# Kernel tuning notes

Hardware: AMD Instinct MI355X
Metric: run time of the kernel (lower is better)

## Reference

```python
import jax, jax.numpy as jnp
import numpy as np

D_MODEL = 1024
NHEAD = 16
HEAD_DIM = D_MODEL // NHEAD


def setup_inputs() -> dict:
    key = jax.random.key(0)
    ks = jax.random.split(key, 9)
    s = 0.02
    x = jax.random.normal(ks[0], (2, 2048, D_MODEL), dtype=jnp.float32)
    Wq = jax.random.normal(ks[1], (D_MODEL, D_MODEL), dtype=jnp.float32) * s
    bq = jnp.zeros((D_MODEL,), jnp.float32)
    Wk = jax.random.normal(ks[2], (D_MODEL, D_MODEL), dtype=jnp.float32) * s
    bk = jnp.zeros((D_MODEL,), jnp.float32)
    Wv = jax.random.normal(ks[3], (D_MODEL, D_MODEL), dtype=jnp.float32) * s
    bv = jnp.zeros((D_MODEL,), jnp.float32)
    Wo = jax.random.normal(ks[4], (D_MODEL, D_MODEL), dtype=jnp.float32) * s
    bo = jnp.zeros((D_MODEL,), jnp.float32)
    return {"x": x, "Wq": Wq, "bq": bq, "Wk": Wk, "bk": bk,
            "Wv": Wv, "bv": bv, "Wo": Wo, "bo": bo}


def _rope(x, sin, cos):
    # x: [B, L, H, Dh]; rotate-half as in the torch module
    half = x.shape[-1] // 2
    x1, x2 = x[..., :half], x[..., half:]
    rotated = jnp.concatenate([-x2, x1], axis=-1)
    return x * cos + rotated * sin


def reference(x, Wq, bq, Wk, bk, Wv, bv, Wo, bo):
    B, L, D = x.shape
    H, Dh = NHEAD, HEAD_DIM
    q = (x @ Wq.T + bq).reshape(B, L, H, Dh)
    k = (x @ Wk.T + bk).reshape(B, L, H, Dh)
    v = (x @ Wv.T + bv).reshape(B, L, H, Dh)

    inv_freq = 1.0 / (10000.0 ** (jnp.arange(0, Dh, 2, dtype=jnp.float32) / Dh))
    t = jnp.arange(L, dtype=jnp.float32)
    freqs = jnp.einsum('i,j->ij', t, inv_freq)          # [L, Dh/2]
    emb = jnp.concatenate([freqs, freqs], axis=-1)      # [L, Dh]
    cos = jnp.cos(emb)[None, :, None, :]
    sin = jnp.sin(emb)[None, :, None, :]

    q = _rope(q, sin, cos)
    k = _rope(k, sin, cos)

    # [B, H, L, L]
    scores = jnp.einsum('bqhd,bkhd->bhqk', q, k) / jnp.sqrt(jnp.float32(Dh))
    attn = jax.nn.softmax(scores, axis=-1)
    # dropout in eval mode = identity (p given as 0.0)
    out = jnp.einsum('bhqk,bkhd->bqhd', attn, v).reshape(B, L, D)
    return out @ Wo.T + bo
```

## Files before the change

### kernel.cpp

```cpp
#include <hip/hip_runtime.h>
#include <math.h>

#define D_MODEL 1024
#define NHEAD 16
#define HEAD_DIM 64
#define L_SEQ 2048
#define BATCH 2
#define M_ROWS 4096
#define SC_Q 0.18033688011112042f

typedef __attribute__((ext_vector_type(8))) short short8;
typedef __attribute__((ext_vector_type(4))) float floatx4;
typedef __attribute__((ext_vector_type(2))) __fp16 half2_t;
typedef __attribute__((ext_vector_type(4))) __fp16 half4_t;
typedef __attribute__((ext_vector_type(8))) __fp16 half8_t;

#if __has_builtin(__builtin_amdgcn_exp2f)
#define EXP2F(x) __builtin_amdgcn_exp2f(x)
#else
#define EXP2F(x) exp2f(x)
#endif

__device__ inline unsigned f2bf_u(float x) {
    unsigned u = __float_as_uint(x);
    return (u + 0x7fffu + ((u >> 16) & 1u)) >> 16;
}

__device__ inline void gl_lds16(const void* g, void* l) {
    __builtin_amdgcn_global_load_lds((const __attribute__((address_space(1))) void*)g,
                                     (__attribute__((address_space(3))) void*)l, 16, 0, 0);
}

__device__ inline void permlane16_swap(unsigned& a, unsigned& b) {
#if __has_builtin(__builtin_amdgcn_permlane16_swap)
    auto r = __builtin_amdgcn_permlane16_swap(a, b, false, false);
    a = r[0];
    b = r[1];
#else
    asm("v_permlane16_swap_b32 %0, %1" : "+v"(a), "+v"(b));
#endif
}

__global__ __launch_bounds__(256) void cvt_all(
    const float* __restrict__ x,  const float* __restrict__ wq,
    const float* __restrict__ wk, const float* __restrict__ wv,
    const float* __restrict__ wo,
    unsigned short* __restrict__ xb,  unsigned short* __restrict__ wqb,
    unsigned short* __restrict__ wkb, unsigned short* __restrict__ wvb,
    unsigned short* __restrict__ wob, float* __restrict__ rt) {
    if (blockIdx.y == 5) {
        for (int idx = blockIdx.x * 256 + threadIdx.x; idx < L_SEQ * 16;
             idx += gridDim.x * 256) {
            int l = idx >> 4, f = idx & 15;
            float if0 = (float)pow(10000.0, -(double)f / 32.0);
            float if1 = (float)pow(10000.0, -(double)(f + 16) / 32.0);
            float s0, c0, s1, c1;
            sincosf((float)l * if0, &s0, &c0);
            sincosf((float)l * if1, &s1, &c1);
            float4 v = {c0, c1, s0, s1};
            *(float4*)(rt + (size_t)idx * 4) = v;
        }
        return;
    }
    const float* s; unsigned short* d; int n;
    switch (blockIdx.y) {
        case 0:  s = x;  d = xb;  n = M_ROWS * D_MODEL; break;
        case 1:  s = wq; d = wqb; n = D_MODEL * D_MODEL; break;
        case 2:  s = wk; d = wkb; n = D_MODEL * D_MODEL; break;
        case 3:  s = wv; d = wvb; n = D_MODEL * D_MODEL; break;
        default: s = wo; d = wob; n = D_MODEL * D_MODEL; break;
    }
    int stride = gridDim.x * 256 * 4;
    for (int i = (blockIdx.x * 256 + threadIdx.x) * 4; i < n; i += stride) {
        float4 v = *(const float4*)(s + i);
        ushort4 o;
        o.x = (unsigned short)f2bf_u(v.x);
        o.y = (unsigned short)f2bf_u(v.y);
        o.z = (unsigned short)f2bf_u(v.z);
        o.w = (unsigned short)f2bf_u(v.w);
        *(ushort4*)(d + i) = o;
    }
}

__global__ __launch_bounds__(256) void gemm_qkv(
    const unsigned short* __restrict__ xb,
    const unsigned short* __restrict__ wqb, const unsigned short* __restrict__ wkb,
    const unsigned short* __restrict__ wvb,
    const float* __restrict__ bq, const float* __restrict__ bk,
    const float* __restrict__ bv, const float* __restrict__ rt,
    unsigned short* __restrict__ qo, unsigned short* __restrict__ ko,
    unsigned short* __restrict__ vo) {
    __shared__ __align__(16) unsigned short As[128 * 32];
    __shared__ __align__(16) unsigned short Bs[128 * 32];

    const int K = D_MODEL;
    const int tid = threadIdx.x;
    const int lane = tid & 63;
    const int w = tid >> 6;
    const int wm = (w & 1) * 64;
    const int wn = (w >> 1) * 64;
    const int m0 = blockIdx.x * 128;
    const int n0 = blockIdx.y * 128;

    const unsigned short* Wsel; const float* bsel;
    unsigned short* osel; int mode; float oscale;
    if (blockIdx.z == 0)      { Wsel = wqb; bsel = bq; osel = qo; mode = 1; oscale = SC_Q; }
    else if (blockIdx.z == 1) { Wsel = wkb; bsel = bk; osel = ko; mode = 1; oscale = 1.0f; }
    else                      { Wsel = wvb; bsel = bv; osel = vo; mode = 2; oscale = 1.0f; }

    floatx4 acc[4][4];
#pragma unroll
    for (int i = 0; i < 4; ++i)
#pragma unroll
        for (int j = 0; j < 4; ++j) acc[i][j] = (floatx4){0.f, 0.f, 0.f, 0.f};

    const int sr = lane >> 2;
    const int ss = lane & 3;
    const unsigned short* Ag = xb + (size_t)m0 * K;
    const unsigned short* Bg = Wsel + (size_t)n0 * K;

    for (int k0 = 0; k0 < K; k0 += 32) {
        __syncthreads();
#pragma unroll
        for (int t = 0; t < 2; ++t) {
            int R0 = t * 64 + w * 16;
            int r = R0 + sr;
            int c = ss ^ ((r >> 1) & 3);
            gl_lds16(Ag + (size_t)r * K + k0 + c * 8, (void*)(As + R0 * 32));
            gl_lds16(Bg + (size_t)r * K + k0 + c * 8, (void*)(Bs + R0 * 32));
        }
        __syncthreads();

        short8 af[4], bf[4];
#pragma unroll
        for (int mt = 0; mt < 4; ++mt) {
            int ar = wm + mt * 16 + (lane & 15);
            int slot = (lane >> 4) ^ ((ar >> 1) & 3);
            af[mt] = *(const short8*)(As + ar * 32 + slot * 8);
        }
#pragma unroll
        for (int nt = 0; nt < 4; ++nt) {
            int br = wn + nt * 16 + (lane & 15);
            int slot = (lane >> 4) ^ ((br >> 1) & 3);
            bf[nt] = *(const short8*)(Bs + br * 32 + slot * 8);
        }
#pragma unroll
        for (int mt = 0; mt < 4; ++mt)
#pragma unroll
            for (int nt = 0; nt < 4; ++nt)
                acc[mt][nt] = __builtin_amdgcn_mfma_f32_16x16x32_bf16(
                    af[mt], bf[nt], acc[mt][nt], 0, 0, 0);
    }

#pragma unroll
    for (int nt = 0; nt < 4; ++nt) {
        float bn = bsel[n0 + wn + nt * 16 + (lane & 15)];
#pragma unroll
        for (int mt = 0; mt < 4; ++mt)
#pragma unroll
            for (int i = 0; i < 4; ++i) acc[mt][nt][i] += bn;
    }

    const int h = (n0 + wn) >> 6;

    if (mode == 1) {
#pragma unroll
        for (int mt = 0; mt < 4; ++mt)
#pragma unroll
            for (int i = 0; i < 4; ++i) {
                int m = m0 + wm + mt * 16 + (lane >> 4) * 4 + i;
                int b = m >> 11, l = m & (L_SEQ - 1);
                float4 tc = *(const float4*)(rt + ((size_t)(l * 16 + (lane & 15)) << 2));
#pragma unroll
                for (int nt = 0; nt < 4; ++nt) {
                    int dh = nt * 16 + (lane & 15);
                    float partner = acc[mt][nt ^ 2][i];
                    float rot = (nt < 2) ? -partner : partner;
                    float c = (nt & 1) ? tc.y : tc.x;
                    float s = (nt & 1) ? tc.w : tc.z;
                    float val = (acc[mt][nt][i] * c + rot * s) * oscale;
                    size_t idx = (((size_t)(b * NHEAD + h)) * L_SEQ + l) * HEAD_DIM + dh;
                    osel[idx] = (unsigned short)f2bf_u(val);
                }
            }
    } else {
#pragma unroll
        for (int mt = 0; mt < 4; ++mt)
#pragma unroll
            for (int ih = 0; ih < 4; ih += 2) {
                int m = m0 + wm + mt * 16 + (lane >> 4) * 4 + ih;
                int b = m >> 11, l = m & (L_SEQ - 1);
#pragma unroll
                for (int nt = 0; nt < 4; ++nt) {
                    int dh = nt * 16 + (lane & 15);
                    union { half2_t h; unsigned u; } cv;
                    cv.h = __builtin_amdgcn_cvt_pkrtz(acc[mt][nt][ih], acc[mt][nt][ih + 1]);
                    size_t idx = (((size_t)(b * NHEAD + h)) * HEAD_DIM + dh) * L_SEQ + l;
                    *(unsigned*)(vo + idx) = cv.u;
                }
            }
    }
}

__global__ __launch_bounds__(256) void gemm_out(
    const unsigned short* __restrict__ A, const unsigned short* __restrict__ Wb,
    const float* __restrict__ bias, float* __restrict__ out) {
    __shared__ __align__(16) unsigned short As[64 * 32];
    __shared__ __align__(16) unsigned short Bs[128 * 32];

    const int K = D_MODEL;
    const int tid = threadIdx.x;
    const int lane = tid & 63;
    const int w = tid >> 6;
    const int wm = (w & 1) * 32;
    const int wn = (w >> 1) * 64;
    const int m0 = blockIdx.x * 64;
    const int n0 = blockIdx.y * 128;

    floatx4 acc[2][4];
#pragma unroll
    for (int i = 0; i < 2; ++i)
#pragma unroll
        for (int j = 0; j < 4; ++j) acc[i][j] = (floatx4){0.f, 0.f, 0.f, 0.f};

    const int sr = lane >> 2;
    const int ss = lane & 3;
    const unsigned short* Ag = A + (size_t)m0 * K;
    const unsigned short* Bg = Wb + (size_t)n0 * K;

    for (int k0 = 0; k0 < K; k0 += 32) {
        __syncthreads();
        {
            int r = w * 16 + sr;
            int c = ss ^ ((r >> 1) & 3);
            gl_lds16(Ag + (size_t)r * K + k0 + c * 8, (void*)(As + (w * 16) * 32));
        }
#pragma unroll
        for (int t = 0; t < 2; ++t) {
            int R0 = t * 64 + w * 16;
            int r = R0 + sr;
            int c = ss ^ ((r >> 1) & 3);
            gl_lds16(Bg + (size_t)r * K + k0 + c * 8, (void*)(Bs + R0 * 32));
        }
        __syncthreads();

        short8 af[2], bf[4];
#pragma unroll
        for (int mt = 0; mt < 2; ++mt) {
            int ar = wm + mt * 16 + (lane & 15);
            int slot = (lane >> 4) ^ ((ar >> 1) & 3);
            af[mt] = *(const short8*)(As + ar * 32 + slot * 8);
        }
#pragma unroll
        for (int nt = 0; nt < 4; ++nt) {
            int br = wn + nt * 16 + (lane & 15);
            int slot = (lane >> 4) ^ ((br >> 1) & 3);
            bf[nt] = *(const short8*)(Bs + br * 32 + slot * 8);
        }
#pragma unroll
        for (int mt = 0; mt < 2; ++mt)
#pragma unroll
            for (int nt = 0; nt < 4; ++nt)
                acc[mt][nt] = __builtin_amdgcn_mfma_f32_16x16x32_bf16(
                    af[mt], bf[nt], acc[mt][nt], 0, 0, 0);
    }

#pragma unroll
    for (int nt = 0; nt < 4; ++nt) {
        int n = n0 + wn + nt * 16 + (lane & 15);
        float bn = bias[n];
#pragma unroll
        for (int mt = 0; mt < 2; ++mt)
#pragma unroll
            for (int i = 0; i < 4; ++i) {
                int m = m0 + wm + mt * 16 + (lane >> 4) * 4 + i;
                out[(size_t)m * D_MODEL + n] = acc[mt][nt][i] + bn;
            }
    }
}

__global__ __launch_bounds__(256, 4) void attn_mfma(
    const unsigned short* __restrict__ q, const unsigned short* __restrict__ k,
    const unsigned short* __restrict__ vt,
    unsigned short* __restrict__ ao) {
    __shared__ __align__(16) unsigned short Ks[128 * 64];
    __shared__ __align__(16) unsigned short Vs[64 * 128];

    const int tid = threadIdx.x;
    const int lane = tid & 63;
    const int w = tid >> 6;
    const int quad = lane >> 4;
    const int ln = lane & 15;

    const int GX = L_SEQ / 128;
    int lin = blockIdx.y * GX + blockIdx.x;
    lin = (lin & 7) * 64 + (lin >> 3);
    const int q0 = (lin & (GX - 1)) * 128;
    const int bh = lin >> 4;

    const unsigned short* qb = q + (size_t)bh * L_SEQ * HEAD_DIM;
    const unsigned short* kb = k + (size_t)bh * L_SEQ * HEAD_DIM;
    const unsigned short* vb = vt + (size_t)bh * HEAD_DIM * L_SEQ;

    short8 qf[2][2];
#pragma unroll
    for (int ntq = 0; ntq < 2; ++ntq)
#pragma unroll
        for (int ks = 0; ks < 2; ++ks)
            qf[ntq][ks] = *(const short8*)(
                qb + (size_t)(q0 + w * 32 + ntq * 16 + ln) * HEAD_DIM
                + ks * 32 + quad * 8);

    floatx4 o[2][4];
    floatx4 ls[2];
#pragma unroll
    for (int ntq = 0; ntq < 2; ++ntq) {
        ls[ntq] = (floatx4){0.f, 0.f, 0.f, 0.f};
#pragma unroll
        for (int j = 0; j < 4; ++j) o[ntq][j] = (floatx4){0.f, 0.f, 0.f, 0.f};
    }

    half8_t ones8;
#pragma unroll
    for (int j = 0; j < 8; ++j) ones8[j] = (__fp16)1.0f;

    const int srk = lane >> 3;
    const int ssk = lane & 7;
    const int srv = lane >> 4;
    const int ssv = lane & 15;
    const int pb = ((quad & 1) << 1) | (quad >> 1);

    for (int t = 0; t < L_SEQ / 128; ++t) {
        int kv0 = t * 128;
        __syncthreads();
#pragma unroll
        for (int tt = 0; tt < 4; ++tt) {
            {
                int R0 = tt * 32 + w * 8;
                int r = R0 + srk;
                int c = ssk ^ (r & 7);
                gl_lds16(kb + (size_t)(kv0 + r) * HEAD_DIM + c * 8, (void*)(Ks + R0 * 64));
            }
            {
                int R0 = tt * 16 + w * 4;
                int r = R0 + srv;
                int c = ssv ^ (r & 15);
                gl_lds16(vb + (size_t)r * L_SEQ + kv0 + c * 8, (void*)(Vs + R0 * 128));
            }
        }
        __syncthreads();

#pragma unroll
        for (int mt2 = 0; mt2 < 4; ++mt2) {
            floatx4 s[2][2];
#pragma unroll
            for (int c = 0; c < 2; ++c) {
                int ar = mt2 * 32 + c * 16 + ln;
                short8 kf0 = *(const short8*)(Ks + ar * 64 + ((quad) ^ (ar & 7)) * 8);
                short8 kf1 = *(const short8*)(Ks + ar * 64 + ((4 + quad) ^ (ar & 7)) * 8);

                floatx4 t0 = (floatx4){0.f, 0.f, 0.f, 0.f};
                floatx4 t1 = (floatx4){0.f, 0.f, 0.f, 0.f};
                t0 = __builtin_amdgcn_mfma_f32_16x16x32_bf16(kf0, qf[0][0], t0, 0, 0, 0);
                t0 = __builtin_amdgcn_mfma_f32_16x16x32_bf16(kf1, qf[0][1], t0, 0, 0, 0);
                t1 = __builtin_amdgcn_mfma_f32_16x16x32_bf16(kf0, qf[1][0], t1, 0, 0, 0);
                t1 = __builtin_amdgcn_mfma_f32_16x16x32_bf16(kf1, qf[1][1], t1, 0, 0, 0);
                s[c][0] = t0;
                s[c][1] = t1;
            }

            half8_t vf[4];
#pragma unroll
            for (int ntd = 0; ntd < 4; ++ntd) {
                int row = ntd * 16 + ln;
                int slot = (mt2 * 4 + pb) ^ (row & 15);
                vf[ntd] = *(const half8_t*)(Vs + row * 128 + slot * 8);
            }

#pragma unroll
            for (int tq = 0; tq < 2; ++tq) {
                union { half2_t h; unsigned u; } c0l, c0h, c1l, c1h;
                c0l.h = __builtin_amdgcn_cvt_pkrtz(EXP2F(s[0][tq][0]), EXP2F(s[0][tq][1]));
                c0h.h = __builtin_amdgcn_cvt_pkrtz(EXP2F(s[0][tq][2]), EXP2F(s[0][tq][3]));
                c1l.h = __builtin_amdgcn_cvt_pkrtz(EXP2F(s[1][tq][0]), EXP2F(s[1][tq][1]));
                c1h.h = __builtin_amdgcn_cvt_pkrtz(EXP2F(s[1][tq][2]), EXP2F(s[1][tq][3]));
                unsigned a0 = c0l.u, b0 = c1l.u;
                unsigned a1 = c0h.u, b1 = c1h.u;
                permlane16_swap(a0, b0);
                permlane16_swap(a1, b1);
                union { half8_t h8; unsigned u[4]; } af;
                af.u[0] = a0; af.u[1] = a1; af.u[2] = b0; af.u[3] = b1;

                ls[tq] = __builtin_amdgcn_mfma_f32_16x16x32_f16(af.h8, ones8, ls[tq], 0, 0, 0);
#pragma unroll
                for (int ntd = 0; ntd < 4; ++ntd)
                    o[tq][ntd] = __builtin_amdgcn_mfma_f32_16x16x32_f16(
                        af.h8, vf[ntd], o[tq][ntd], 0, 0, 0);
            }
        }
    }

    const int b = bh >> 4, h = bh & (NHEAD - 1);
#pragma unroll
    for (int ntq = 0; ntq < 2; ++ntq)
#pragma unroll
        for (int i = 0; i < 4; ++i) {
            int l = q0 + w * 32 + ntq * 16 + quad * 4 + i;
            float inv = 1.0f / ls[ntq][i];
#pragma unroll
            for (int ntd = 0; ntd < 4; ++ntd) {
                int dh = ntd * 16 + ln;
                size_t idx = ((size_t)b * L_SEQ + l) * D_MODEL + h * HEAD_DIM + dh;
                ao[idx] = (unsigned short)f2bf_u(o[ntq][ntd][i] * inv);
            }
        }
}

extern "C" void kernel_launch(void* const* d_in, const int* in_sizes, int n_in,
                              void* d_out, int out_size, void* d_ws, size_t ws_size,
                              hipStream_t stream) {
    const float* x  = (const float*)d_in[0];
    const float* Wq = (const float*)d_in[1];
    const float* bq = (const float*)d_in[2];
    const float* Wk = (const float*)d_in[3];
    const float* bk = (const float*)d_in[4];
    const float* Wv = (const float*)d_in[5];
    const float* bv = (const float*)d_in[6];
    const float* Wo = (const float*)d_in[7];
    const float* bo = (const float*)d_in[8];
    float* outp = (float*)d_out;

    const size_t XE = (size_t)M_ROWS * D_MODEL;
    const size_t WE = (size_t)D_MODEL * D_MODEL;
    unsigned short* wqb = (unsigned short*)d_ws;
    unsigned short* wkb = wqb + WE;
    unsigned short* wvb = wkb + WE;
    unsigned short* wob = wvb + WE;
    unsigned short* qbf = wob + WE;
    unsigned short* kbf = qbf + XE;
    unsigned short* vtb = kbf + XE;
    unsigned short* xb  = vtb + XE;
    unsigned short* aob = xb;
    float* rt    = (float*)(xb + XE);

    cvt_all<<<dim3(1024, 6), 256, 0, stream>>>(x, Wq, Wk, Wv, Wo,
                                               xb, wqb, wkb, wvb, wob, rt);

    gemm_qkv<<<dim3(M_ROWS / 128, D_MODEL / 128, 3), 256, 0, stream>>>(
        xb, wqb, wkb, wvb, bq, bk, bv, rt, qbf, kbf, vtb);

    attn_mfma<<<dim3(L_SEQ / 128, BATCH * NHEAD), 256, 0, stream>>>(
        qbf, kbf, vtb, aob);

    gemm_out<<<dim3(M_ROWS / 64, D_MODEL / 128), 256, 0, stream>>>(aob, wob, bo, outp);
}
```

Before: 188.9 us.

## Use two waves per attention block with 64 query rows per wave

The attention kernel now launches 128 threads (2 waves) instead of 256, and each wave processes 64 query rows instead of 32. Each K fragment loaded from LDS is reused across four query tiles, and each V fragment across four, halving LDS reads per MFMA. The cost is higher register pressure (twice the accumulators and Q fragments) and fewer waves per block to hide latency, with each wave doing more of the global-to-LDS loading.

```diff
diff --git a/kernel.cpp b/kernel.cpp
--- a/kernel.cpp
+++ b/kernel.cpp
@@ -279,7 +279,7 @@
     }
 }
 
-__global__ __launch_bounds__(256, 4) void attn_mfma(
+__global__ __launch_bounds__(128, 2) void attn_mfma(
     const unsigned short* __restrict__ q, const unsigned short* __restrict__ k,
     const unsigned short* __restrict__ vt,
     unsigned short* __restrict__ ao) {
@@ -302,19 +302,19 @@
     const unsigned short* kb = k + (size_t)bh * L_SEQ * HEAD_DIM;
     const unsigned short* vb = vt + (size_t)bh * HEAD_DIM * L_SEQ;
 
-    short8 qf[2][2];
-#pragma unroll
-    for (int ntq = 0; ntq < 2; ++ntq)
+    short8 qf[4][2];
+#pragma unroll
+    for (int ntq = 0; ntq < 4; ++ntq)
 #pragma unroll
         for (int ks = 0; ks < 2; ++ks)
             qf[ntq][ks] = *(const short8*)(
-                qb + (size_t)(q0 + w * 32 + ntq * 16 + ln) * HEAD_DIM
+                qb + (size_t)(q0 + w * 64 + ntq * 16 + ln) * HEAD_DIM
                 + ks * 32 + quad * 8);
 
-    floatx4 o[2][4];
-    floatx4 ls[2];
-#pragma unroll
-    for (int ntq = 0; ntq < 2; ++ntq) {
+    floatx4 o[4][4];
+    floatx4 ls[4];
+#pragma unroll
+    for (int ntq = 0; ntq < 4; ++ntq) {
         ls[ntq] = (floatx4){0.f, 0.f, 0.f, 0.f};
 #pragma unroll
         for (int j = 0; j < 4; ++j) o[ntq][j] = (floatx4){0.f, 0.f, 0.f, 0.f};
@@ -331,18 +331,18 @@
     const int pb = ((quad & 1) << 1) | (quad >> 1);
 
     for (int t = 0; t < L_SEQ / 128; ++t) {
-        int kv0 = t * 128;
-        __syncthreads();
-#pragma unroll
-        for (int tt = 0; tt < 4; ++tt) {
+        const int kv0 = t * 128;
+        __syncthreads();
+#pragma unroll
+        for (int tt = 0; tt < 8; ++tt) {
             {
-                int R0 = tt * 32 + w * 8;
+                int R0 = tt * 16 + w * 8;
                 int r = R0 + srk;
                 int c = ssk ^ (r & 7);
                 gl_lds16(kb + (size_t)(kv0 + r) * HEAD_DIM + c * 8, (void*)(Ks + R0 * 64));
             }
             {
-                int R0 = tt * 16 + w * 4;
+                int R0 = tt * 8 + w * 4;
                 int r = R0 + srv;
                 int c = ssv ^ (r & 15);
                 gl_lds16(vb + (size_t)r * L_SEQ + kv0 + c * 8, (void*)(Vs + R0 * 128));
@@ -352,21 +352,12 @@
 
 #pragma unroll
         for (int mt2 = 0; mt2 < 4; ++mt2) {
-            floatx4 s[2][2];
+            short8 kf0[2], kf1[2];
 #pragma unroll
             for (int c = 0; c < 2; ++c) {
                 int ar = mt2 * 32 + c * 16 + ln;
-                short8 kf0 = *(const short8*)(Ks + ar * 64 + ((quad) ^ (ar & 7)) * 8);
-                short8 kf1 = *(const short8*)(Ks + ar * 64 + ((4 + quad) ^ (ar & 7)) * 8);
-
-                floatx4 t0 = (floatx4){0.f, 0.f, 0.f, 0.f};
-                floatx4 t1 = (floatx4){0.f, 0.f, 0.f, 0.f};
-                t0 = __builtin_amdgcn_mfma_f32_16x16x32_bf16(kf0, qf[0][0], t0, 0, 0, 0);
-                t0 = __builtin_amdgcn_mfma_f32_16x16x32_bf16(kf1, qf[0][1], t0, 0, 0, 0);
-                t1 = __builtin_amdgcn_mfma_f32_16x16x32_bf16(kf0, qf[1][0], t1, 0, 0, 0);
-                t1 = __builtin_amdgcn_mfma_f32_16x16x32_bf16(kf1, qf[1][1], t1, 0, 0, 0);
-                s[c][0] = t0;
-                s[c][1] = t1;
+                kf0[c] = *(const short8*)(Ks + ar * 64 + ((quad) ^ (ar & 7)) * 8);
+                kf1[c] = *(const short8*)(Ks + ar * 64 + ((4 + quad) ^ (ar & 7)) * 8);
             }
 
             half8_t vf[4];
@@ -378,34 +369,51 @@
             }
 
 #pragma unroll
-            for (int tq = 0; tq < 2; ++tq) {
-                union { half2_t h; unsigned u; } c0l, c0h, c1l, c1h;
-                c0l.h = __builtin_amdgcn_cvt_pkrtz(EXP2F(s[0][tq][0]), EXP2F(s[0][tq][1]));
-                c0h.h = __builtin_amdgcn_cvt_pkrtz(EXP2F(s[0][tq][2]), EXP2F(s[0][tq][3]));
-                c1l.h = __builtin_amdgcn_cvt_pkrtz(EXP2F(s[1][tq][0]), EXP2F(s[1][tq][1]));
-                c1h.h = __builtin_amdgcn_cvt_pkrtz(EXP2F(s[1][tq][2]), EXP2F(s[1][tq][3]));
-                unsigned a0 = c0l.u, b0 = c1l.u;
-                unsigned a1 = c0h.u, b1 = c1h.u;
-                permlane16_swap(a0, b0);
-                permlane16_swap(a1, b1);
-                union { half8_t h8; unsigned u[4]; } af;
-                af.u[0] = a0; af.u[1] = a1; af.u[2] = b0; af.u[3] = b1;
-
-                ls[tq] = __builtin_amdgcn_mfma_f32_16x16x32_f16(af.h8, ones8, ls[tq], 0, 0, 0);
-#pragma unroll
-                for (int ntd = 0; ntd < 4; ++ntd)
-                    o[tq][ntd] = __builtin_amdgcn_mfma_f32_16x16x32_f16(
-                        af.h8, vf[ntd], o[tq][ntd], 0, 0, 0);
+            for (int p = 0; p < 2; ++p) {
+                floatx4 s[2][2];
+#pragma unroll
+                for (int c = 0; c < 2; ++c) {
+                    floatx4 t0 = (floatx4){0.f, 0.f, 0.f, 0.f};
+                    floatx4 t1 = (floatx4){0.f, 0.f, 0.f, 0.f};
+                    t0 = __builtin_amdgcn_mfma_f32_16x16x32_bf16(kf0[c], qf[2 * p + 0][0], t0, 0, 0, 0);
+                    t0 = __builtin_amdgcn_mfma_f32_16x16x32_bf16(kf1[c], qf[2 * p + 0][1], t0, 0, 0, 0);
+                    t1 = __builtin_amdgcn_mfma_f32_16x16x32_bf16(kf0[c], qf[2 * p + 1][0], t1, 0, 0, 0);
+                    t1 = __builtin_amdgcn_mfma_f32_16x16x32_bf16(kf1[c], qf[2 * p + 1][1], t1, 0, 0, 0);
+                    s[c][0] = t0;
+                    s[c][1] = t1;
+                }
+
+#pragma unroll
+                for (int tq2 = 0; tq2 < 2; ++tq2) {
+                    const int tq = 2 * p + tq2;
+                    union { half2_t h; unsigned u; } c0l, c0h, c1l, c1h;
+                    c0l.h = __builtin_amdgcn_cvt_pkrtz(EXP2F(s[0][tq2][0]), EXP2F(s[0][tq2][1]));
+                    c0h.h = __builtin_amdgcn_cvt_pkrtz(EXP2F(s[0][tq2][2]), EXP2F(s[0][tq2][3]));
+                    c1l.h = __builtin_amdgcn_cvt_pkrtz(EXP2F(s[1][tq2][0]), EXP2F(s[1][tq2][1]));
+                    c1h.h = __builtin_amdgcn_cvt_pkrtz(EXP2F(s[1][tq2][2]), EXP2F(s[1][tq2][3]));
+                    unsigned a0 = c0l.u, b0 = c1l.u;
+                    unsigned a1 = c0h.u, b1 = c1h.u;
+                    permlane16_swap(a0, b0);
+                    permlane16_swap(a1, b1);
+                    union { half8_t h8; unsigned u[4]; } af;
+                    af.u[0] = a0; af.u[1] = a1; af.u[2] = b0; af.u[3] = b1;
+
+                    ls[tq] = __builtin_amdgcn_mfma_f32_16x16x32_f16(af.h8, ones8, ls[tq], 0, 0, 0);
+#pragma unroll
+                    for (int ntd = 0; ntd < 4; ++ntd)
+                        o[tq][ntd] = __builtin_amdgcn_mfma_f32_16x16x32_f16(
+                            af.h8, vf[ntd], o[tq][ntd], 0, 0, 0);
+                }
             }
         }
     }
 
     const int b = bh >> 4, h = bh & (NHEAD - 1);
 #pragma unroll
-    for (int ntq = 0; ntq < 2; ++ntq)
+    for (int ntq = 0; ntq < 4; ++ntq)
 #pragma unroll
         for (int i = 0; i < 4; ++i) {
-            int l = q0 + w * 32 + ntq * 16 + quad * 4 + i;
+            int l = q0 + w * 64 + ntq * 16 + quad * 4 + i;
             float inv = 1.0f / ls[ntq][i];
 #pragma unroll
             for (int ntd = 0; ntd < 4; ++ntd) {
@@ -449,7 +457,7 @@
     gemm_qkv<<<dim3(M_ROWS / 128, D_MODEL / 128, 3), 256, 0, stream>>>(
         xb, wqb, wkb, wvb, bq, bk, bv, rt, qbf, kbf, vtb);
 
-    attn_mfma<<<dim3(L_SEQ / 128, BATCH * NHEAD), 256, 0, stream>>>(
+    attn_mfma<<<dim3(L_SEQ / 128, BATCH * NHEAD), 128, 0, stream>>>(
         qbf, kbf, vtb, aob);
 
     gemm_out<<<dim3(M_ROWS / 64, D_MODEL / 128), 256, 0, stream>>>(aob, wob, bo, outp);
```

New measurement: 204.5 us. 8.3% more time.
